# Kernel tuning notes

Hardware: AMD Instinct MI355X
Metric: run time of the kernel (lower is better)

## Reference

```python
import jax, jax.numpy as jnp
import numpy as np

IN_F = 128
OUT_F = 64


def _xavier(key, shape, gain=1.414):
    fan_in, fan_out = shape[0], shape[1]
    bound = gain * np.sqrt(6.0 / (fan_in + fan_out))
    return jax.random.uniform(key, shape, jnp.float32, -bound, bound)


def setup_inputs() -> dict:
    key = jax.random.key(0)
    ks = jax.random.split(key, 11)
    features = jax.random.normal(ks[0], (2, 32, 2048, IN_F), dtype=jnp.float32)
    d = {"features": features}
    for i in range(4):
        d[f"W{i+1}"] = _xavier(ks[1 + 2 * i], (IN_F, 2 * OUT_F))
        d[f"a{i+1}"] = _xavier(ks[2 + 2 * i], (2 * OUT_F, 1))
    d["Wo"] = _xavier(ks[9], (8 * OUT_F, OUT_F))
    return d


def _head(features, W, a):
    # features: [b,g,n,i]; W: [i,j]; a: [j,1]
    Wx = jnp.einsum('bgni,ij->bgnj', features, W)          # [b,g,n,2F]
    att = jax.nn.softmax(Wx @ a, axis=2)                   # softmax over nodes, [b,g,n,1]
    return jnp.einsum('bgno,bgnj->bgj', att, Wx)           # pooled [b,g,2F]


def reference(features, W1, a1, W2, a2, W3, a3, W4, a4, Wo):
    h1 = _head(features, W1, a1)
    h2 = _head(features, W2, a2)
    h3 = _head(features, W3, a3)
    h4 = _head(features, W4, a4)
    multi = jnp.concatenate([h1, h2, h3, h4], axis=2)      # [b,g,8F]
    return jax.nn.elu(multi @ Wo)                          # [b,g,F]
```

## Files before the change

### kernel.cpp

```cpp
#include <hip/hip_runtime.h>
#include <math.h>

#define BG     64
#define NN     2048
#define F      128
#define OUTF   64
#define NSLICE 16
#define SNODES 128

#define OFF_WEFF 0
#define OFF_FP   512
#define OFF_LP   (512 + BG * NSLICE * 4 * F)

template <int CTRL>
__device__ __forceinline__ float dpp_add(float x) {
  int y = __builtin_amdgcn_update_dpp(0, __float_as_int(x), CTRL, 0xF, 0xF, true);
  return x + __int_as_float(y);
}
__device__ __forceinline__ float rowsum16(float x) {
  x = dpp_add<0x121>(x);
  x = dpp_add<0x122>(x);
  x = dpp_add<0x124>(x);
  x = dpp_add<0x128>(x);
  return x;
}
__device__ __forceinline__ float dot8(float4 a0, float4 a1, float4 b0, float4 b1) {
  return a0.x * b0.x + a0.y * b0.y + a0.z * b0.z + a0.w * b0.w +
         a1.x * b1.x + a1.y * b1.y + a1.z * b1.z + a1.w * b1.w;
}

__global__ __launch_bounds__(256) void k_weff(
    const float* __restrict__ W1, const float* __restrict__ a1,
    const float* __restrict__ W2, const float* __restrict__ a2,
    const float* __restrict__ W3, const float* __restrict__ a3,
    const float* __restrict__ W4, const float* __restrict__ a4,
    float* __restrict__ ws) {
  int h = blockIdx.x, t = threadIdx.x;
  const float* W = (h == 0) ? W1 : (h == 1) ? W2 : (h == 2) ? W3 : W4;
  const float* a = (h == 0) ? a1 : (h == 1) ? a2 : (h == 2) ? a3 : a4;
  __shared__ float aL[F];
  __shared__ float part[F][33];

  if (t < F) aL[t] = a[t];
  __syncthreads();

  int c = t & 31, r8 = t >> 5;
#pragma unroll
  for (int it = 0; it < 16; ++it) {
    int row = it * 8 + r8;
    float4 w = ((const float4*)(W + row * F))[c];
    part[row][c] = w.x * aL[4 * c] + w.y * aL[4 * c + 1] +
                   w.z * aL[4 * c + 2] + w.w * aL[4 * c + 3];
  }
  __syncthreads();

  if (t < F) {
    float s = 0.f;
#pragma unroll
    for (int c2 = 0; c2 < 32; ++c2) s += part[t][c2];
    ws[OFF_WEFF + h * F + t] = s;
  }
}

__global__ __launch_bounds__(256) void k_main(
    const float* __restrict__ feat, float* __restrict__ ws) {
  int g = blockIdx.x >> 4;
  int slice = blockIdx.x & (NSLICE - 1);
  int t = threadIdx.x;
  int r = t >> 4;
  int c8 = t & 15;

  const float4* wp = (const float4*)(ws + OFF_WEFF);
  float4 w4[4][2];
#pragma unroll
  for (int h = 0; h < 4; ++h) {
    w4[h][0] = wp[h * 32 + c8 * 2 + 0];
    w4[h][1] = wp[h * 32 + c8 * 2 + 1];
  }

  const float4* fb =
      (const float4*)(feat + ((size_t)g * NN + slice * SNODES) * F);

  float4 acc[4][2];
#pragma unroll
  for (int h = 0; h < 4; ++h) {
    acc[h][0] = make_float4(0.f, 0.f, 0.f, 0.f);
    acc[h][1] = make_float4(0.f, 0.f, 0.f, 0.f);
  }
  float4 se = make_float4(0.f, 0.f, 0.f, 0.f);

#pragma unroll
  for (int kk = 0; kk < 2; ++kk) {
    float4 ld[4][2];
#pragma unroll
    for (int b = 0; b < 4; ++b) {
      int nl = (kk * 4 + b) * 16 + r;
      ld[b][0] = fb[nl * 32 + c8 * 2 + 0];
      ld[b][1] = fb[nl * 32 + c8 * 2 + 1];
    }
#pragma unroll
    for (int b = 0; b < 4; ++b) {
      float px = dot8(ld[b][0], ld[b][1], w4[0][0], w4[0][1]);
      float py = dot8(ld[b][0], ld[b][1], w4[1][0], w4[1][1]);
      float pz = dot8(ld[b][0], ld[b][1], w4[2][0], w4[2][1]);
      float pw = dot8(ld[b][0], ld[b][1], w4[3][0], w4[3][1]);
      px = rowsum16(px); py = rowsum16(py);
      pz = rowsum16(pz); pw = rowsum16(pw);
      float4 e = make_float4(__expf(px), __expf(py), __expf(pz), __expf(pw));
      se.x += e.x; se.y += e.y; se.z += e.z; se.w += e.w;
#pragma unroll
      for (int h = 0; h < 4; ++h) {
        float eh = (h == 0) ? e.x : (h == 1) ? e.y : (h == 2) ? e.z : e.w;
        acc[h][0].x += eh * ld[b][0].x; acc[h][0].y += eh * ld[b][0].y;
        acc[h][0].z += eh * ld[b][0].z; acc[h][0].w += eh * ld[b][0].w;
        acc[h][1].x += eh * ld[b][1].x; acc[h][1].y += eh * ld[b][1].y;
        acc[h][1].z += eh * ld[b][1].z; acc[h][1].w += eh * ld[b][1].w;
      }
    }
  }

  __shared__ float4 red[4][16][33];
  __shared__ float4 seR[16];
#pragma unroll
  for (int h = 0; h < 4; ++h) {
    red[h][r][c8 * 2 + 0] = acc[h][0];
    red[h][r][c8 * 2 + 1] = acc[h][1];
  }
  if (c8 == 0) seR[r] = se;
  __syncthreads();

  if (t < 128) {
    int h = t >> 5, c4 = t & 31;
    float4 s = make_float4(0.f, 0.f, 0.f, 0.f);
#pragma unroll
    for (int rr = 0; rr < 16; ++rr) {
      float4 v = red[h][rr][c4];
      s.x += v.x; s.y += v.y; s.z += v.z; s.w += v.w;
    }
    ((float4*)(ws + OFF_FP))[(size_t)(g * NSLICE + slice) * 128 + h * 32 + c4] = s;
  }
  if (t == 0) {
    float4 L = make_float4(0.f, 0.f, 0.f, 0.f);
#pragma unroll
    for (int rr = 0; rr < 16; ++rr) {
      float4 v = seR[rr];
      L.x += v.x; L.y += v.y; L.z += v.z; L.w += v.w;
    }
    ((float4*)(ws + OFF_LP))[g * NSLICE + slice] = L;
  }
}

__global__ __launch_bounds__(256) void k_final(
    const float* __restrict__ W1, const float* __restrict__ W2,
    const float* __restrict__ W3, const float* __restrict__ W4,
    const float* __restrict__ Wo, const float* __restrict__ ws,
    float* __restrict__ out) {
  int g = blockIdx.x;
  int t = threadIdx.x;

  __shared__ float4 f4[896];
  __shared__ float invl[4];
  float* fbuf = (float*)f4;

  const float4* FP4 = (const float4*)(ws + OFF_FP) + (size_t)g * NSLICE * 128;

  if (t < 4) {
    float s = 0.f;
#pragma unroll
    for (int sl = 0; sl < NSLICE; ++sl)
      s += ws[OFF_LP + (g * NSLICE + sl) * 4 + t];
    invl[t] = 1.0f / s;
  }
  {
    int j = t & 127, half = t >> 7;
    float4 s4 = make_float4(0.f, 0.f, 0.f, 0.f);
#pragma unroll
    for (int sl = 0; sl < 8; ++sl) {
      float4 v = FP4[(size_t)(half * 8 + sl) * 128 + j];
      s4.x += v.x; s4.y += v.y; s4.z += v.z; s4.w += v.w;
    }
    f4[half * 128 + j] = s4;
  }
  __syncthreads();
  if (t < 128) {
    float4 a = f4[t], b = f4[128 + t];
    float inv = invl[t >> 5];
    f4[256 + t] = make_float4((a.x + b.x) * inv, (a.y + b.y) * inv,
                              (a.z + b.z) * inv, (a.w + b.w) * inv);
  }
  __syncthreads();

  {
    int c = t & 31, rg = (t >> 5) & 1, h = t >> 6;
    const float* Wsel = (h == 0) ? W1 : (h == 1) ? W2 : (h == 2) ? W3 : W4;
    const float4* W4p = (const float4*)Wsel;
    const float* fph = fbuf + 1024 + h * F;
    float4 acc = make_float4(0.f, 0.f, 0.f, 0.f);
#pragma unroll 8
    for (int k = 0; k < 64; ++k) {
      int i = rg * 64 + k;
      float s = fph[i];
      float4 w = W4p[i * 32 + c];
      acc.x += s * w.x; acc.y += s * w.y; acc.z += s * w.z; acc.w += s * w.w;
    }
    f4[512 + (h * 2 + rg) * 32 + c] = acc;
  }
  __syncthreads();
  if (t < 128) {
    int h = t >> 5, c = t & 31;
    float4 a = f4[512 + (h * 2) * 32 + c];
    float4 b = f4[512 + (h * 2 + 1) * 32 + c];
    f4[768 + h * 32 + c] = make_float4(a.x + b.x, a.y + b.y,
                                       a.z + b.z, a.w + b.w);
  }
  __syncthreads();

  {
    int o4 = t & 15, rg = t >> 4;
    const float4* Wo4 = (const float4*)Wo;
    const float* mu = fbuf + 3072;
    float4 acc = make_float4(0.f, 0.f, 0.f, 0.f);
#pragma unroll 8
    for (int k = 0; k < 32; ++k) {
      int i = rg * 32 + k;
      float s = mu[i];
      float4 w = Wo4[i * 16 + o4];
      acc.x += s * w.x; acc.y += s * w.y; acc.z += s * w.z; acc.w += s * w.w;
    }
    f4[rg * 16 + o4] = acc;
  }
  __syncthreads();
  if (t < OUTF) {
    float s = 0.f;
#pragma unroll
    for (int rg = 0; rg < 16; ++rg) s += fbuf[rg * 64 + t];
    out[g * OUTF + t] = (s > 0.f) ? s : expm1f(s);
  }
}

extern "C" void kernel_launch(void* const* d_in, const int* in_sizes, int n_in,
                              void* d_out, int out_size, void* d_ws, size_t ws_size,
                              hipStream_t stream) {
  const float* feat = (const float*)d_in[0];
  const float* W1 = (const float*)d_in[1];
  const float* a1 = (const float*)d_in[2];
  const float* W2 = (const float*)d_in[3];
  const float* a2 = (const float*)d_in[4];
  const float* W3 = (const float*)d_in[5];
  const float* a3 = (const float*)d_in[6];
  const float* W4 = (const float*)d_in[7];
  const float* a4 = (const float*)d_in[8];
  const float* Wo = (const float*)d_in[9];
  float* ws = (float*)d_ws;
  float* out = (float*)d_out;

  k_weff<<<4, 256, 0, stream>>>(W1, a1, W2, a2, W3, a3, W4, a4, ws);
  k_main<<<BG * NSLICE, 256, 0, stream>>>(feat, ws);
  k_final<<<BG, 256, 0, stream>>>(W1, W2, W3, W4, Wo, ws, out);
}
```

Measured before the change: 125.1 us.

## Split nodes into more slices and use 32-lane rows per node

Raises the slice count per group from 16 to 64 (32 nodes each), so the main kernel launches four times as many blocks. Each node row is now read by 32 lanes holding one float4 each, reduced with DPP plus ds_swizzle, instead of 16 lanes holding two float4s. The aim is more memory-level parallelism and better occupancy on the bandwidth-bound feature stream. The cost is four times more partial sums for the final kernel to read and reduce, plus fewer loads in flight per thread.

```diff
diff --git a/kernel.cpp b/kernel.cpp
--- a/kernel.cpp
+++ b/kernel.cpp
@@ -5,8 +5,8 @@
 #define NN     2048
 #define F      128
 #define OUTF   64
-#define NSLICE 16
-#define SNODES 128
+#define NSLICE 64
+#define SNODES 32
 
 #define OFF_WEFF 0
 #define OFF_FP   512
@@ -24,9 +24,14 @@
   x = dpp_add<0x128>(x);
   return x;
 }
-__device__ __forceinline__ float dot8(float4 a0, float4 a1, float4 b0, float4 b1) {
-  return a0.x * b0.x + a0.y * b0.y + a0.z * b0.z + a0.w * b0.w +
-         a1.x * b1.x + a1.y * b1.y + a1.z * b1.z + a1.w * b1.w;
+__device__ __forceinline__ float sum32(float x) {
+  x = rowsum16(x);
+  float y = __int_as_float(
+      __builtin_amdgcn_ds_swizzle(__float_as_int(x), 0x401F));
+  return x + y;
+}
+__device__ __forceinline__ float dot4(float4 a, float4 b) {
+  return a.x * b.x + a.y * b.y + a.z * b.z + a.w * b.w;
 }
 
 __global__ __launch_bounds__(256) void k_weff(
@@ -62,88 +67,73 @@
   }
 }
 
-__global__ __launch_bounds__(256) void k_main(
+__global__ __launch_bounds__(256, 4) void k_main(
     const float* __restrict__ feat, float* __restrict__ ws) {
-  int g = blockIdx.x >> 4;
+  int g = blockIdx.x >> 6;
   int slice = blockIdx.x & (NSLICE - 1);
   int t = threadIdx.x;
-  int r = t >> 4;
-  int c8 = t & 15;
+  int c  = t & 31;
+  int q  = (t >> 5) & 1;
+  int wv = t >> 6;
 
   const float4* wp = (const float4*)(ws + OFF_WEFF);
-  float4 w4[4][2];
-#pragma unroll
-  for (int h = 0; h < 4; ++h) {
-    w4[h][0] = wp[h * 32 + c8 * 2 + 0];
-    w4[h][1] = wp[h * 32 + c8 * 2 + 1];
-  }
+  float4 w4[4];
+#pragma unroll
+  for (int h = 0; h < 4; ++h) w4[h] = wp[h * 32 + c];
 
   const float4* fb =
       (const float4*)(feat + ((size_t)g * NN + slice * SNODES) * F);
 
-  float4 acc[4][2];
-#pragma unroll
-  for (int h = 0; h < 4; ++h) {
-    acc[h][0] = make_float4(0.f, 0.f, 0.f, 0.f);
-    acc[h][1] = make_float4(0.f, 0.f, 0.f, 0.f);
-  }
+  float4 ld[4];
+#pragma unroll
+  for (int p = 0; p < 4; ++p) {
+    int n = p * 8 + wv * 2 + q;
+    ld[p] = fb[n * 32 + c];
+  }
+
+  float4 acc[4];
+#pragma unroll
+  for (int h = 0; h < 4; ++h) acc[h] = make_float4(0.f, 0.f, 0.f, 0.f);
   float4 se = make_float4(0.f, 0.f, 0.f, 0.f);
 
 #pragma unroll
-  for (int kk = 0; kk < 2; ++kk) {
-    float4 ld[4][2];
-#pragma unroll
-    for (int b = 0; b < 4; ++b) {
-      int nl = (kk * 4 + b) * 16 + r;
-      ld[b][0] = fb[nl * 32 + c8 * 2 + 0];
-      ld[b][1] = fb[nl * 32 + c8 * 2 + 1];
-    }
-#pragma unroll
-    for (int b = 0; b < 4; ++b) {
-      float px = dot8(ld[b][0], ld[b][1], w4[0][0], w4[0][1]);
-      float py = dot8(ld[b][0], ld[b][1], w4[1][0], w4[1][1]);
-      float pz = dot8(ld[b][0], ld[b][1], w4[2][0], w4[2][1]);
-      float pw = dot8(ld[b][0], ld[b][1], w4[3][0], w4[3][1]);
-      px = rowsum16(px); py = rowsum16(py);
-      pz = rowsum16(pz); pw = rowsum16(pw);
-      float4 e = make_float4(__expf(px), __expf(py), __expf(pz), __expf(pw));
-      se.x += e.x; se.y += e.y; se.z += e.z; se.w += e.w;
-#pragma unroll
-      for (int h = 0; h < 4; ++h) {
-        float eh = (h == 0) ? e.x : (h == 1) ? e.y : (h == 2) ? e.z : e.w;
-        acc[h][0].x += eh * ld[b][0].x; acc[h][0].y += eh * ld[b][0].y;
-        acc[h][0].z += eh * ld[b][0].z; acc[h][0].w += eh * ld[b][0].w;
-        acc[h][1].x += eh * ld[b][1].x; acc[h][1].y += eh * ld[b][1].y;
-        acc[h][1].z += eh * ld[b][1].z; acc[h][1].w += eh * ld[b][1].w;
-      }
-    }
-  }
-
-  __shared__ float4 red[4][16][33];
-  __shared__ float4 seR[16];
-#pragma unroll
-  for (int h = 0; h < 4; ++h) {
-    red[h][r][c8 * 2 + 0] = acc[h][0];
-    red[h][r][c8 * 2 + 1] = acc[h][1];
-  }
-  if (c8 == 0) seR[r] = se;
+  for (int p = 0; p < 4; ++p) {
+    float4 f = ld[p];
+    float s0 = sum32(dot4(f, w4[0]));
+    float s1 = sum32(dot4(f, w4[1]));
+    float s2 = sum32(dot4(f, w4[2]));
+    float s3 = sum32(dot4(f, w4[3]));
+    float e0 = __expf(s0), e1 = __expf(s1), e2 = __expf(s2), e3 = __expf(s3);
+    se.x += e0; se.y += e1; se.z += e2; se.w += e3;
+    acc[0].x += e0 * f.x; acc[0].y += e0 * f.y; acc[0].z += e0 * f.z; acc[0].w += e0 * f.w;
+    acc[1].x += e1 * f.x; acc[1].y += e1 * f.y; acc[1].z += e1 * f.z; acc[1].w += e1 * f.w;
+    acc[2].x += e2 * f.x; acc[2].y += e2 * f.y; acc[2].z += e2 * f.z; acc[2].w += e2 * f.w;
+    acc[3].x += e3 * f.x; acc[3].y += e3 * f.y; acc[3].z += e3 * f.z; acc[3].w += e3 * f.w;
+  }
+
+  __shared__ float4 red[4][8][33];
+  __shared__ float4 seR[8];
+  int grp = wv * 2 + q;
+#pragma unroll
+  for (int h = 0; h < 4; ++h) red[h][grp][c] = acc[h];
+  if (c == 0) seR[grp] = se;
   __syncthreads();
 
   if (t < 128) {
-    int h = t >> 5, c4 = t & 31;
+    int h = t >> 5, cc = t & 31;
     float4 s = make_float4(0.f, 0.f, 0.f, 0.f);
 #pragma unroll
-    for (int rr = 0; rr < 16; ++rr) {
-      float4 v = red[h][rr][c4];
+    for (int gg = 0; gg < 8; ++gg) {
+      float4 v = red[h][gg][cc];
       s.x += v.x; s.y += v.y; s.z += v.z; s.w += v.w;
     }
-    ((float4*)(ws + OFF_FP))[(size_t)(g * NSLICE + slice) * 128 + h * 32 + c4] = s;
+    ((float4*)(ws + OFF_FP))[(size_t)(g * NSLICE + slice) * 128 + h * 32 + cc] = s;
   }
   if (t == 0) {
     float4 L = make_float4(0.f, 0.f, 0.f, 0.f);
 #pragma unroll
-    for (int rr = 0; rr < 16; ++rr) {
-      float4 v = seR[rr];
+    for (int gg = 0; gg < 8; ++gg) {
+      float4 v = seR[gg];
       L.x += v.x; L.y += v.y; L.z += v.z; L.w += v.w;
     }
     ((float4*)(ws + OFF_LP))[g * NSLICE + slice] = L;
@@ -175,8 +165,8 @@
     int j = t & 127, half = t >> 7;
     float4 s4 = make_float4(0.f, 0.f, 0.f, 0.f);
 #pragma unroll
-    for (int sl = 0; sl < 8; ++sl) {
-      float4 v = FP4[(size_t)(half * 8 + sl) * 128 + j];
+    for (int sl = 0; sl < 32; ++sl) {
+      float4 v = FP4[(size_t)(half * 32 + sl) * 128 + j];
       s4.x += v.x; s4.y += v.y; s4.z += v.z; s4.w += v.w;
     }
     f4[half * 128 + j] = s4;
```

Result: faster. 118.7 us (median of 2 runs) (-5.2%).
